# Optimization experiments

Hardware: AMD Instinct MI355X
Metric: run time of the kernel (lower is better)

Reference implementation:

```python
import jax, jax.numpy as jnp
import numpy as np

D_MODEL = 2048
NUM_HEADS = 16
NUM_KV_HEADS = 4
HEAD_DIM = D_MODEL // NUM_HEADS
ROPE_THETA = 10000.0


def setup_inputs() -> dict:
    key = jax.random.key(0)
    ks = jax.random.split(key, 5)
    B, S = 2, 2048
    scale = 0.02
    return {
        "x": jax.random.normal(ks[0], (B, S, D_MODEL), dtype=jnp.float32),
        "wq": jax.random.normal(ks[1], (D_MODEL, NUM_HEADS * HEAD_DIM), dtype=jnp.float32) * scale,
        "wk": jax.random.normal(ks[2], (D_MODEL, NUM_KV_HEADS * HEAD_DIM), dtype=jnp.float32) * scale,
        "wv": jax.random.normal(ks[3], (D_MODEL, NUM_KV_HEADS * HEAD_DIM), dtype=jnp.float32) * scale,
        "wo": jax.random.normal(ks[4], (NUM_HEADS * HEAD_DIM, D_MODEL), dtype=jnp.float32) * scale,
    }


def _rope_cos_sin(seq_len, head_dim, dtype):
    # Llama-style: freqs over even indices, angles = pos * inv_freq
    inv_freq = 1.0 / (ROPE_THETA ** (jnp.arange(0, head_dim, 2, dtype=jnp.float32) / head_dim))
    ang = jnp.arange(seq_len, dtype=jnp.float32)[:, None] * inv_freq[None, :]  # [S, hd/2]
    cos = jnp.cos(ang).astype(dtype)[None, :, None, :]  # [1,S,1,hd/2]
    sin = jnp.sin(ang).astype(dtype)[None, :, None, :]
    return cos, sin


def _apply_rope(x, cos, sin):
    # x: [B,S,H,hd]; interleaved complex rotation on pairs (x[2i], x[2i+1])
    x1 = x[..., 0::2]
    x2 = x[..., 1::2]
    y1 = x1 * cos - x2 * sin
    y2 = x1 * sin + x2 * cos
    return jnp.stack([y1, y2], axis=-1).reshape(x.shape)


def reference(x, wq, wk, wv, wo):
    B, S, D = x.shape
    H, KV, hd = NUM_HEADS, NUM_KV_HEADS, HEAD_DIM
    g = H // KV
    q = (x @ wq).reshape(B, S, H, hd)
    k = (x @ wk).reshape(B, S, KV, hd)
    v = (x @ wv).reshape(B, S, KV, hd)
    cos, sin = _rope_cos_sin(S, hd, x.dtype)
    q = _apply_rope(q, cos, sin)
    k = _apply_rope(k, cos, sin)
    q = q.transpose(0, 2, 1, 3)  # [B,H,S,hd]
    k = k.transpose(0, 2, 1, 3)  # [B,KV,S,hd]
    v = v.transpose(0, 2, 1, 3)
    k = jnp.repeat(k, g, axis=1)  # GQA: [B,H,S,hd]
    v = jnp.repeat(v, g, axis=1)
    attn = jnp.einsum('bqsh,bqlh->bqsl', q, k) * (1.0 / np.sqrt(hd)).astype(np.float32)
    attn = jax.nn.softmax(attn, axis=-1)  # non-causal, as in source
    out = jnp.einsum('bqsl,bqlh->bqsh', attn, v)
    out = out.transpose(0, 2, 1, 3).reshape(B, S, D)
    return out @ wo
```

## Files before the change

### kernel.cpp

```cpp
#include <hip/hip_runtime.h>


typedef __attribute__((ext_vector_type(8))) short short8;
typedef __attribute__((ext_vector_type(4))) float f32x4;

#define DEV static __device__ __forceinline__

#define NB 2
#define NS 2048
#define ND 2048
#define NH 16
#define NKV 4
#define HD 128
#define NQKV 3072

DEV unsigned short f2bf(float f) {
  union { float f; unsigned u; } v; v.f = f;
  unsigned r = v.u + 0x7fffu + ((v.u >> 16) & 1u);
  return (unsigned short)(r >> 16);
}
DEV unsigned short f2bf_fast(float f) {
  union { float f; unsigned u; } v; v.f = f;
  return (unsigned short)((v.u + 0x8000u) >> 16);
}
DEV float bf2f(unsigned short u) {
  union { unsigned u; float f; } v; v.u = ((unsigned)u) << 16; return v.f;
}

typedef const __attribute__((address_space(1))) void* gas1_t;
typedef __attribute__((address_space(3))) void* las3_t;
DEV void gload16(const void* g, void* l) {
  __builtin_amdgcn_global_load_lds((gas1_t)g, (las3_t)l, 16, 0, 0);
}

DEV f32x4 mfma16(short8 a, short8 b, f32x4 c) {
  return __builtin_amdgcn_mfma_f32_16x16x32_bf16(a, b, c, 0, 0, 0);
}


__global__ __launch_bounds__(256) void convert_x_kernel(const float* __restrict__ x,
                                                        unsigned short* __restrict__ xb) {
  size_t i = ((size_t)blockIdx.x * 256 + threadIdx.x) * 4;
  float4 v = *(const float4*)(x + i);
  unsigned long long pack = (unsigned long long)f2bf(v.x)
                          | ((unsigned long long)f2bf(v.y) << 16)
                          | ((unsigned long long)f2bf(v.z) << 32)
                          | ((unsigned long long)f2bf(v.w) << 48);
  *(unsigned long long*)(xb + i) = pack;
}

__global__ __launch_bounds__(256) void transpose_w_kernel(const float* __restrict__ src,
                                                          unsigned short* __restrict__ dst,
                                                          int K, int N) {
  __shared__ float tile[64][65];
  const int k0 = blockIdx.x * 64, n0 = blockIdx.y * 64;
  for (int i = threadIdx.x; i < 4096; i += 256) {
    int r = i >> 6, c = i & 63;
    tile[r][c] = src[(size_t)(k0 + r) * N + n0 + c];
  }
  __syncthreads();
  for (int i = threadIdx.x; i < 4096; i += 256) {
    int r = i >> 6, c = i & 63;
    dst[(size_t)(n0 + r) * K + k0 + c] = f2bf(tile[c][r]);
  }
}

__global__ __launch_bounds__(256) void rope_table_kernel(float2* __restrict__ tab) {
  int t = blockIdx.x * 256 + threadIdx.x;
  int s = t >> 6, i = t & 63;
  float freq = powf(10000.0f, -(float)i * (1.0f / 64.0f));
  float ang = (float)s * freq;
  tab[t] = make_float2(cosf(ang), sinf(ang));
}

__global__ __launch_bounds__(256) void rope_scatter_kernel(const unsigned short* __restrict__ QKV,
                                                           const float2* __restrict__ tab,
                                                           unsigned short* __restrict__ Qb,
                                                           unsigned short* __restrict__ Kb) {
  int t = blockIdx.x * 256 + threadIdx.x;
  const float qscale = 0.12751741161895452f;
  if (t < (1 << 22)) {
    int i = t & 63, h = (t >> 6) & 15, s = (t >> 10) & 2047, b = t >> 21;
    const unsigned short* p = QKV + (size_t)(b * NS + s) * NQKV + h * HD + 2 * i;
    float2 cs = tab[s * 64 + i];
    float x1 = bf2f(p[0]), x2 = bf2f(p[1]);
    unsigned short* q = Qb + (size_t)((b * NH + h) * NS + s) * HD + 2 * i;
    q[0] = f2bf((x1 * cs.x - x2 * cs.y) * qscale);
    q[1] = f2bf((x1 * cs.y + x2 * cs.x) * qscale);
  } else {
    int u = t - (1 << 22);
    int i = u & 63, kv = (u >> 6) & 3, s = (u >> 8) & 2047, b = u >> 19;
    const unsigned short* p = QKV + (size_t)(b * NS + s) * NQKV + 2048 + kv * HD + 2 * i;
    float2 cs = tab[s * 64 + i];
    float x1 = bf2f(p[0]), x2 = bf2f(p[1]);
    unsigned short* k = Kb + (size_t)((b * NKV + kv) * NS + s) * HD + 2 * i;
    k[0] = f2bf(x1 * cs.x - x2 * cs.y);
    k[1] = f2bf(x1 * cs.y + x2 * cs.x);
  }
}

__global__ __launch_bounds__(256) void transpose_v_kernel(const unsigned short* __restrict__ QKV,
                                                          unsigned short* __restrict__ Vt) {
  __shared__ unsigned short tile[64][65];
  const int bk = blockIdx.x, b = bk >> 2, kv = bk & 3;
  const int s0 = blockIdx.y * 64, d0 = blockIdx.z * 64;
  for (int i = threadIdx.x; i < 4096; i += 256) {
    int r = i >> 6, c = i & 63;
    tile[r][c] = QKV[(size_t)(b * NS + s0 + r) * NQKV + 2560 + kv * HD + d0 + c];
  }
  __syncthreads();
  for (int i = threadIdx.x; i < 4096; i += 256) {
    int r = i >> 6, c = i & 63;
    Vt[(size_t)((b * NKV + kv) * HD + d0 + r) * NS + s0 + c] = tile[c][r];
  }
}


template <int N, bool OUTBF16>
__global__ __launch_bounds__(256) void gemm_kernel(const unsigned short* __restrict__ A,
                                                   const unsigned short* __restrict__ Bt,
                                                   void* __restrict__ Cout) {
  __shared__ unsigned short As[128 * 32];
  __shared__ unsigned short Bs[128 * 32];
  const int K = 2048;
  const int tid = threadIdx.x, wid = tid >> 6, lane = tid & 63;
  const int wm = wid >> 1, wn = wid & 1;
  const int m0 = blockIdx.x * 128, n0 = blockIdx.y * 128;
  f32x4 acc[4][4] = {};
  const int srow = tid >> 2;
  const int scol = (tid & 3) * 8;
  const unsigned short* Ab = A + (size_t)(m0 + srow) * K + scol;
  const unsigned short* Ab2 = Ab + (size_t)64 * K;
  const unsigned short* Bb = Bt + (size_t)(n0 + srow) * K + scol;
  const unsigned short* Bb2 = Bb + (size_t)64 * K;

  for (int kt = 0; kt < K; kt += 32) {
    gload16(Ab + kt, &As[wid * 512]);
    gload16(Ab2 + kt, &As[2048 + wid * 512]);
    gload16(Bb + kt, &Bs[wid * 512]);
    gload16(Bb2 + kt, &Bs[2048 + wid * 512]);
    __syncthreads();
    short8 af[4], bfr[4];
#pragma unroll
    for (int r = 0; r < 4; ++r)
      af[r] = *(const short8*)&As[(wm * 64 + r * 16 + (lane & 15)) * 32 + (lane >> 4) * 8];
#pragma unroll
    for (int c = 0; c < 4; ++c)
      bfr[c] = *(const short8*)&Bs[(wn * 64 + c * 16 + (lane & 15)) * 32 + (lane >> 4) * 8];
    __builtin_amdgcn_s_setprio(1);
#pragma unroll
    for (int r = 0; r < 4; ++r)
#pragma unroll
      for (int c = 0; c < 4; ++c)
        acc[r][c] = mfma16(af[r], bfr[c], acc[r][c]);
    __builtin_amdgcn_s_setprio(0);
    __syncthreads();
  }

  if (OUTBF16) {
    unsigned short* C = (unsigned short*)Cout;
#pragma unroll
    for (int r = 0; r < 4; ++r) {
      const int row = m0 + wm * 64 + r * 16 + (lane >> 4) * 4;
#pragma unroll
      for (int c = 0; c < 4; ++c) {
        const int col = n0 + wn * 64 + c * 16 + (lane & 15);
#pragma unroll
        for (int j = 0; j < 4; ++j)
          C[(size_t)(row + j) * N + col] = f2bf(acc[r][c][j]);
      }
    }
  } else {
    float* C = (float*)Cout;
#pragma unroll
    for (int r = 0; r < 4; ++r) {
      const int row = m0 + wm * 64 + r * 16 + (lane >> 4) * 4;
#pragma unroll
      for (int c = 0; c < 4; ++c) {
        const int col = n0 + wn * 64 + c * 16 + (lane & 15);
#pragma unroll
        for (int j = 0; j < 4; ++j)
          C[(size_t)(row + j) * N + col] = acc[r][c][j];
      }
    }
  }
}


__global__ __launch_bounds__(256, 2) void attn_kernel(const unsigned short* __restrict__ Qb,
                                                      const unsigned short* __restrict__ Kb,
                                                      const unsigned short* __restrict__ Vt,
                                                      unsigned short* __restrict__ O) {
  __shared__ unsigned short Ks[2][64 * 128];
  __shared__ unsigned short Vs[2][128 * 64];
  __shared__ unsigned short Ps[4][32 * 64];
  const int tid = threadIdx.x, wid = tid >> 6, lane = tid & 63;
  const int blk = blockIdx.x;
  const int qt = blk & 15, h = (blk >> 4) & 15, b = blk >> 8;
  const int kvh = h >> 2;
  const int q0 = qt * 128 + wid * 32;

  const unsigned short* qhead = Qb + (size_t)((b * NH + h) * NS) * HD;
  const unsigned short* khead = Kb + (size_t)((b * NKV + kvh) * NS) * HD;
  const unsigned short* vhead = Vt + (size_t)((b * NKV + kvh) * HD) * NS;

  const int cl = lane & 15, g4 = (lane >> 4) * 4, hi8 = (lane >> 4) * 8;
  const int swk = (lane & 7) << 3;

  auto stageKV = [&](int buf, int kt) {
#pragma unroll
    for (int i = 0; i < 4; ++i) {
      int row = i * 16 + (tid >> 4);
      int col = ((tid & 15) * 8) ^ ((row & 7) << 3);
      gload16(khead + (size_t)(kt + row) * HD + col, &Ks[buf][i * 2048 + wid * 512]);
    }
#pragma unroll
    for (int i = 0; i < 4; ++i) {
      int row = i * 32 + (tid >> 3);
      int col = ((tid & 7) * 8) ^ ((row & 7) << 3);
      gload16(vhead + (size_t)row * NS + kt + col, &Vs[buf][i * 2048 + wid * 512]);
    }
  };

  stageKV(0, 0);

  short8 qf[2][4];
#pragma unroll
  for (int r = 0; r < 2; ++r)
#pragma unroll
    for (int kk = 0; kk < 4; ++kk)
      qf[r][kk] = *(const short8*)(qhead + (size_t)(q0 + r * 16 + cl) * HD + kk * 32 + hi8);

  f32x4 od[2][8] = {};
  float mrun[2][4], lpart[2][4];
#pragma unroll
  for (int r = 0; r < 2; ++r)
#pragma unroll
    for (int j = 0; j < 4; ++j) { mrun[r][j] = -1e30f; lpart[r][j] = 0.0f; }

  int cur = 0;
  for (int it = 0; it < NS / 64; ++it) {
    if (it + 1 < NS / 64) {
      stageKV(cur ^ 1, (it + 1) * 64);
      asm volatile("s_waitcnt vmcnt(8)" ::: "memory");
    } else {
      asm volatile("s_waitcnt vmcnt(0)" ::: "memory");
    }
    __builtin_amdgcn_s_barrier();

    const unsigned short* ks = Ks[cur];
    const unsigned short* vs = Vs[cur];

    f32x4 s[2][4];
#pragma unroll
    for (int r = 0; r < 2; ++r)
#pragma unroll
      for (int c4 = 0; c4 < 4; ++c4) s[r][c4] = f32x4{0.f, 0.f, 0.f, 0.f};
    __builtin_amdgcn_s_setprio(1);
#pragma unroll
    for (int c4 = 0; c4 < 4; ++c4)
#pragma unroll
      for (int kk = 0; kk < 4; ++kk) {
        short8 kf = *(const short8*)&ks[((c4 * 16 + cl) * 128 + kk * 32 + hi8) ^ swk];
        s[0][c4] = mfma16(qf[0][kk], kf, s[0][c4]);
        s[1][c4] = mfma16(qf[1][kk], kf, s[1][c4]);
      }
    __builtin_amdgcn_s_setprio(0);

    float mt[2][4];
#pragma unroll
    for (int r = 0; r < 2; ++r)
#pragma unroll
      for (int j = 0; j < 4; ++j) {
        float m = fmaxf(fmaxf(s[r][0][j], s[r][1][j]), fmaxf(s[r][2][j], s[r][3][j]));
#pragma unroll
        for (int msk = 1; msk <= 8; msk <<= 1)
          m = fmaxf(m, __shfl_xor(m, msk, 64));
        mt[r][j] = m;
      }
    bool need = false;
#pragma unroll
    for (int r = 0; r < 2; ++r)
#pragma unroll
      for (int j = 0; j < 4; ++j)
        need = need || (mt[r][j] > mrun[r][j] + 8.0f);
    if (__any(need)) {
#pragma unroll
      for (int r = 0; r < 2; ++r)
#pragma unroll
        for (int j = 0; j < 4; ++j) {
          float mn = fmaxf(mrun[r][j], mt[r][j]);
          float corr = __builtin_amdgcn_exp2f(mrun[r][j] - mn);
          mrun[r][j] = mn;
          lpart[r][j] *= corr;
#pragma unroll
          for (int c = 0; c < 8; ++c)
            od[r][c][j] *= corr;
        }
    }
#pragma unroll
    for (int r = 0; r < 2; ++r)
#pragma unroll
      for (int j = 0; j < 4; ++j) {
        float acc = 0.f;
#pragma unroll
        for (int c4 = 0; c4 < 4; ++c4) {
          float p = __builtin_amdgcn_exp2f(s[r][c4][j] - mrun[r][j]);
          s[r][c4][j] = p;
          acc += p;
        }
        lpart[r][j] += acc;
      }

    {
      unsigned short* pw = &Ps[wid][0];
#pragma unroll
      for (int r = 0; r < 2; ++r)
#pragma unroll
        for (int j = 0; j < 4; ++j) {
          const int row = r * 16 + g4 + j;
          const int sw = (row & 7) << 3;
#pragma unroll
          for (int c4 = 0; c4 < 4; ++c4)
            pw[(row * 64 + c4 * 16 + cl) ^ sw] = f2bf_fast(s[r][c4][j]);
        }
    }
    asm volatile("s_waitcnt lgkmcnt(0)" ::: "memory");
    __builtin_amdgcn_sched_barrier(0);
    short8 pa[2][2];
#pragma unroll
    for (int r = 0; r < 2; ++r) {
      pa[r][0] = *(const short8*)&Ps[wid][((r * 16 + cl) * 64 + hi8) ^ swk];
      pa[r][1] = *(const short8*)&Ps[wid][((r * 16 + cl) * 64 + 32 + hi8) ^ swk];
    }

    __builtin_amdgcn_s_setprio(1);
#pragma unroll
    for (int c = 0; c < 8; ++c) {
      const int rr = c * 16 + cl;
      short8 vf0 = *(const short8*)&vs[(rr * 64 + hi8) ^ swk];
      short8 vf1 = *(const short8*)&vs[(rr * 64 + 32 + hi8) ^ swk];
      od[0][c] = mfma16(pa[0][0], vf0, od[0][c]);
      od[0][c] = mfma16(pa[0][1], vf1, od[0][c]);
      od[1][c] = mfma16(pa[1][0], vf0, od[1][c]);
      od[1][c] = mfma16(pa[1][1], vf1, od[1][c]);
    }
    __builtin_amdgcn_s_setprio(0);
    __builtin_amdgcn_s_barrier();
    cur ^= 1;
  }

  float linv[2][4];
#pragma unroll
  for (int r = 0; r < 2; ++r)
#pragma unroll
    for (int j = 0; j < 4; ++j) {
      float l = lpart[r][j];
#pragma unroll
      for (int msk = 1; msk <= 8; msk <<= 1)
        l += __shfl_xor(l, msk, 64);
      linv[r][j] = 1.0f / l;
    }
#pragma unroll
  for (int r = 0; r < 2; ++r) {
    const int orow0 = b * NS + q0 + r * 16 + g4;
#pragma unroll
    for (int c = 0; c < 8; ++c)
#pragma unroll
      for (int j = 0; j < 4; ++j)
        O[(size_t)(orow0 + j) * ND + h * HD + c * 16 + cl] = f2bf(od[r][c][j] * linv[r][j]);
  }
}


extern "C" void kernel_launch(void* const* d_in, const int* in_sizes, int n_in,
                              void* d_out, int out_size, void* d_ws, size_t ws_size,
                              hipStream_t stream) {
  const float* x  = (const float*)d_in[0];
  const float* wq = (const float*)d_in[1];
  const float* wk = (const float*)d_in[2];
  const float* wv = (const float*)d_in[3];
  const float* wo = (const float*)d_in[4];
  float* out = (float*)d_out;
  char* ws = (char*)d_ws;

  unsigned short* xb   = (unsigned short*)(ws + 0);
  unsigned short* wT   = (unsigned short*)(ws + 16777216);
  unsigned short* woT  = (unsigned short*)(ws + 29360128);
  float2*         tab  = (float2*)(ws + 37748736);
  unsigned short* QKV  = (unsigned short*)(ws + 38797312);
  unsigned short* Qb   = xb;
  unsigned short* Kb   = wT;
  unsigned short* Vt   = (unsigned short*)(ws + 16777216 + 4194304);
  unsigned short* Obuf = QKV;

  convert_x_kernel<<<8192, 256, 0, stream>>>(x, xb);
  transpose_w_kernel<<<dim3(32, 32), 256, 0, stream>>>(wq, wT, 2048, 2048);
  transpose_w_kernel<<<dim3(32, 8),  256, 0, stream>>>(wk, wT + (size_t)2048 * 2048, 2048, 512);
  transpose_w_kernel<<<dim3(32, 8),  256, 0, stream>>>(wv, wT + (size_t)2560 * 2048, 2048, 512);
  transpose_w_kernel<<<dim3(32, 32), 256, 0, stream>>>(wo, woT, 2048, 2048);
  rope_table_kernel<<<512, 256, 0, stream>>>(tab);

  gemm_kernel<NQKV, true><<<dim3(32, 24), 256, 0, stream>>>(xb, wT, QKV);

  rope_scatter_kernel<<<20480, 256, 0, stream>>>(QKV, tab, Qb, Kb);
  transpose_v_kernel<<<dim3(8, 32, 2), 256, 0, stream>>>(QKV, Vt);

  attn_kernel<<<512, 256, 0, stream>>>(Qb, Kb, Vt, Obuf);

  gemm_kernel<ND, false><<<dim3(32, 16), 256, 0, stream>>>(Obuf, woT, out);
}
```

Measured before the change: 269.6 us.

## Transpose attention MFMAs and keep P in registers via permlane swaps

Swaps the MFMA operand order so S and O are computed transposed, with each lane holding one query row's values. Row max and sum then need fewer cross-lane shuffles, and P is converted to bf16 operand fragments in registers using v_permlane32/16_swap instead of round-tripping through LDS. This removes the per-iteration P LDS writes and reads and the lgkmcnt wait, and the output is written as packed 8-byte stores. The cost is permlane instructions and a different accumulator layout, which must match the MFMA fragment ordering to stay correct.

```diff
diff --git a/kernel.cpp b/kernel.cpp
--- a/kernel.cpp
+++ b/kernel.cpp
@@ -25,6 +25,19 @@
 }
 DEV float bf2f(unsigned short u) {
   union { unsigned u; float f; } v; v.u = ((unsigned)u) << 16; return v.f;
+}
+DEV unsigned pack2bf(float a, float b) {
+  return (unsigned)f2bf_fast(a) | ((unsigned)f2bf_fast(b) << 16);
+}
+DEV unsigned pack2bf_rne(float a, float b) {
+  return (unsigned)f2bf(a) | ((unsigned)f2bf(b) << 16);
+}
+
+DEV void swap32(unsigned &x, unsigned &y) {
+  asm volatile("v_permlane32_swap_b32 %0, %1" : "+v"(x), "+v"(y));
+}
+DEV void swap16(unsigned &x, unsigned &y) {
+  asm volatile("v_permlane16_swap_b32 %0, %1" : "+v"(x), "+v"(y));
 }
 
 typedef const __attribute__((address_space(1))) void* gas1_t;
@@ -193,7 +206,6 @@
                                                       unsigned short* __restrict__ O) {
   __shared__ unsigned short Ks[2][64 * 128];
   __shared__ unsigned short Vs[2][128 * 64];
-  __shared__ unsigned short Ps[4][32 * 64];
   const int tid = threadIdx.x, wid = tid >> 6, lane = tid & 63;
   const int blk = blockIdx.x;
   const int qt = blk & 15, h = (blk >> 4) & 15, b = blk >> 8;
@@ -232,11 +244,7 @@
       qf[r][kk] = *(const short8*)(qhead + (size_t)(q0 + r * 16 + cl) * HD + kk * 32 + hi8);
 
   f32x4 od[2][8] = {};
-  float mrun[2][4], lpart[2][4];
-#pragma unroll
-  for (int r = 0; r < 2; ++r)
-#pragma unroll
-    for (int j = 0; j < 4; ++j) { mrun[r][j] = -1e30f; lpart[r][j] = 0.0f; }
+  float mrun[2] = {-1e30f, -1e30f}, lpart[2] = {0.f, 0.f};
 
   int cur = 0;
   for (int it = 0; it < NS / 64; ++it) {
@@ -262,76 +270,64 @@
 #pragma unroll
       for (int kk = 0; kk < 4; ++kk) {
         short8 kf = *(const short8*)&ks[((c4 * 16 + cl) * 128 + kk * 32 + hi8) ^ swk];
-        s[0][c4] = mfma16(qf[0][kk], kf, s[0][c4]);
-        s[1][c4] = mfma16(qf[1][kk], kf, s[1][c4]);
+        s[0][c4] = mfma16(kf, qf[0][kk], s[0][c4]);
+        s[1][c4] = mfma16(kf, qf[1][kk], s[1][c4]);
       }
     __builtin_amdgcn_s_setprio(0);
 
-    float mt[2][4];
-#pragma unroll
-    for (int r = 0; r < 2; ++r)
-#pragma unroll
-      for (int j = 0; j < 4; ++j) {
-        float m = fmaxf(fmaxf(s[r][0][j], s[r][1][j]), fmaxf(s[r][2][j], s[r][3][j]));
-#pragma unroll
-        for (int msk = 1; msk <= 8; msk <<= 1)
-          m = fmaxf(m, __shfl_xor(m, msk, 64));
-        mt[r][j] = m;
+    float mt[2];
+#pragma unroll
+    for (int r = 0; r < 2; ++r) {
+      float m = fmaxf(fmaxf(fmaxf(s[r][0][0], s[r][0][1]), fmaxf(s[r][0][2], s[r][0][3])),
+                      fmaxf(fmaxf(s[r][1][0], s[r][1][1]), fmaxf(s[r][1][2], s[r][1][3])));
+      float m2 = fmaxf(fmaxf(fmaxf(s[r][2][0], s[r][2][1]), fmaxf(s[r][2][2], s[r][2][3])),
+                       fmaxf(fmaxf(s[r][3][0], s[r][3][1]), fmaxf(s[r][3][2], s[r][3][3])));
+      m = fmaxf(m, m2);
+      m = fmaxf(m, __shfl_xor(m, 16, 64));
+      m = fmaxf(m, __shfl_xor(m, 32, 64));
+      mt[r] = m;
+    }
+    bool need = (mt[0] > mrun[0] + 8.0f) || (mt[1] > mrun[1] + 8.0f);
+    if (__any(need)) {
+#pragma unroll
+      for (int r = 0; r < 2; ++r) {
+        float mn = fmaxf(mrun[r], mt[r]);
+        float corr = __builtin_amdgcn_exp2f(mrun[r] - mn);
+        mrun[r] = mn;
+        lpart[r] *= corr;
+#pragma unroll
+        for (int c = 0; c < 8; ++c)
+          od[r][c] *= corr;
       }
-    bool need = false;
-#pragma unroll
-    for (int r = 0; r < 2; ++r)
-#pragma unroll
-      for (int j = 0; j < 4; ++j)
-        need = need || (mt[r][j] > mrun[r][j] + 8.0f);
-    if (__any(need)) {
-#pragma unroll
-      for (int r = 0; r < 2; ++r)
+    }
+#pragma unroll
+    for (int r = 0; r < 2; ++r) {
+      float acc = 0.f;
+#pragma unroll
+      for (int c4 = 0; c4 < 4; ++c4)
 #pragma unroll
         for (int j = 0; j < 4; ++j) {
-          float mn = fmaxf(mrun[r][j], mt[r][j]);
-          float corr = __builtin_amdgcn_exp2f(mrun[r][j] - mn);
-          mrun[r][j] = mn;
-          lpart[r][j] *= corr;
-#pragma unroll
-          for (int c = 0; c < 8; ++c)
-            od[r][c][j] *= corr;
-        }
-    }
-#pragma unroll
-    for (int r = 0; r < 2; ++r)
-#pragma unroll
-      for (int j = 0; j < 4; ++j) {
-        float acc = 0.f;
-#pragma unroll
-        for (int c4 = 0; c4 < 4; ++c4) {
-          float p = __builtin_amdgcn_exp2f(s[r][c4][j] - mrun[r][j]);
+          float p = __builtin_amdgcn_exp2f(s[r][c4][j] - mrun[r]);
           s[r][c4][j] = p;
           acc += p;
         }
-        lpart[r][j] += acc;
-      }
-
-    {
-      unsigned short* pw = &Ps[wid][0];
-#pragma unroll
-      for (int r = 0; r < 2; ++r)
-#pragma unroll
-        for (int j = 0; j < 4; ++j) {
-          const int row = r * 16 + g4 + j;
-          const int sw = (row & 7) << 3;
-#pragma unroll
-          for (int c4 = 0; c4 < 4; ++c4)
-            pw[(row * 64 + c4 * 16 + cl) ^ sw] = f2bf_fast(s[r][c4][j]);
-        }
-    }
-    asm volatile("s_waitcnt lgkmcnt(0)" ::: "memory");
-    __builtin_amdgcn_sched_barrier(0);
-    short8 pa[2][2];
+      lpart[r] += acc;
+    }
+
+    short8 pb[2][2];
 #pragma unroll
     for (int r = 0; r < 2; ++r) {
-      pa[r][0] = *(const short8*)&Ps[wid][((r * 16 + cl) * 64 + hi8) ^ swk];
-      pa[r][1] = *(const short8*)&Ps[wid][((r * 16 + cl) * 64 + 32 + hi8) ^ swk];
+      unsigned w00 = pack2bf(s[r][0][0], s[r][0][1]), w01 = pack2bf(s[r][0][2], s[r][0][3]);
+      unsigned w10 = pack2bf(s[r][1][0], s[r][1][1]), w11 = pack2bf(s[r][1][2], s[r][1][3]);
+      unsigned w20 = pack2bf(s[r][2][0], s[r][2][1]), w21 = pack2bf(s[r][2][2], s[r][2][3]);
+      unsigned w30 = pack2bf(s[r][3][0], s[r][3][1]), w31 = pack2bf(s[r][3][2], s[r][3][3]);
+      union { unsigned u[4]; short8 v; } t0, t1;
+      swap32(w00, w10); swap16(w00, w10); t0.u[0] = w00; t0.u[2] = w10;
+      swap32(w01, w11); swap16(w01, w11); t0.u[1] = w01; t0.u[3] = w11;
+      swap32(w20, w30); swap16(w20, w30); t1.u[0] = w20; t1.u[2] = w30;
+      swap32(w21, w31); swap16(w21, w31); t1.u[1] = w21; t1.u[3] = w31;
+      pb[r][0] = t0.v;
+      pb[r][1] = t1.v;
     }
 
     __builtin_amdgcn_s_setprio(1);
@@ -340,35 +336,34 @@
       const int rr = c * 16 + cl;
       short8 vf0 = *(const short8*)&vs[(rr * 64 + hi8) ^ swk];
       short8 vf1 = *(const short8*)&vs[(rr * 64 + 32 + hi8) ^ swk];
-      od[0][c] = mfma16(pa[0][0], vf0, od[0][c]);
-      od[0][c] = mfma16(pa[0][1], vf1, od[0][c]);
-      od[1][c] = mfma16(pa[1][0], vf0, od[1][c]);
-      od[1][c] = mfma16(pa[1][1], vf1, od[1][c]);
+      od[0][c] = mfma16(vf0, pb[0][0], od[0][c]);
+      od[0][c] = mfma16(vf1, pb[0][1], od[0][c]);
+      od[1][c] = mfma16(vf0, pb[1][0], od[1][c]);
+      od[1][c] = mfma16(vf1, pb[1][1], od[1][c]);
     }
     __builtin_amdgcn_s_setprio(0);
     __builtin_amdgcn_s_barrier();
     cur ^= 1;
   }
 
-  float linv[2][4];
-#pragma unroll
-  for (int r = 0; r < 2; ++r)
-#pragma unroll
-    for (int j = 0; j < 4; ++j) {
-      float l = lpart[r][j];
-#pragma unroll
-      for (int msk = 1; msk <= 8; msk <<= 1)
-        l += __shfl_xor(l, msk, 64);
-      linv[r][j] = 1.0f / l;
-    }
+  float linv[2];
 #pragma unroll
   for (int r = 0; r < 2; ++r) {
-    const int orow0 = b * NS + q0 + r * 16 + g4;
-#pragma unroll
-    for (int c = 0; c < 8; ++c)
-#pragma unroll
-      for (int j = 0; j < 4; ++j)
-        O[(size_t)(orow0 + j) * ND + h * HD + c * 16 + cl] = f2bf(od[r][c][j] * linv[r][j]);
+    float l = lpart[r];
+    l += __shfl_xor(l, 16, 64);
+    l += __shfl_xor(l, 32, 64);
+    linv[r] = 1.0f / l;
+  }
+#pragma unroll
+  for (int r = 0; r < 2; ++r) {
+    const size_t row = (size_t)(b * NS + q0 + 16 * r + cl);
+#pragma unroll
+    for (int c = 0; c < 8; ++c) {
+      uint2 pk;
+      pk.x = pack2bf_rne(od[r][c][0] * linv[r], od[r][c][1] * linv[r]);
+      pk.y = pack2bf_rne(od[r][c][2] * linv[r], od[r][c][3] * linv[r]);
+      *(uint2*)(O + row * ND + h * HD + c * 16 + g4) = pk;
+    }
   }
 }
 
```

Measured after the change: 248.4 us. 1.09x faster.
